# Performance work log

Hardware: AMD Instinct MI355X
Metric: run time of the kernel (lower is better)

The kernel has to match this reference:

```python
import jax, jax.numpy as jnp
import numpy as np

D = 128      # dim_emb
FF = 512     # dim_ff
H = 8        # nb_heads
HD = D // H
NLE = 2      # encoder layers (action and state)
NLD = 2      # decoder layers
NS = 1       # num_state_encoder
TANH_CLIP = 10.0
BIG = jnp.float32(1e9)


def layer_norm(h, g, b):
    mu = jnp.mean(h, -1, keepdims=True)
    v = jnp.var(h, -1, keepdims=True)
    return g * (h - mu) * jax.lax.rsqrt(v + 1e-5) + b


def mha_self(h, Wq, Wk, Wv, Wo, bq, bk, bv, bo):
    B, S, _ = h.shape
    q = (h @ Wq + bq).reshape(B, S, H, HD)
    k = (h @ Wk + bk).reshape(B, S, H, HD)
    v = (h @ Wv + bv).reshape(B, S, H, HD)
    a = jax.nn.softmax(jnp.einsum('bqhd,bkhd->bhqk', q, k) / np.float32(np.sqrt(HD)), axis=-1)
    return jnp.einsum('bhqk,bkhd->bqhd', a, v).reshape(B, S, D) @ Wo + bo


def encode(tok, Wemb, bemb, aW, aB, W1, b1, W2, b2, ln):
    # tok: [B, S, 2] raw coordinates -> [B, S, D]
    h = tok @ Wemb + bemb
    for l in range(NLE):
        h = layer_norm(h + mha_self(h, *aW[l], *aB[l]), ln[l, 0, 0], ln[l, 0, 1])
        ffo = jax.nn.relu(h @ W1[l] + b1[l]) @ W2[l] + b2[l]
        h = layer_norm(h + ffo, ln[l, 1, 0], ln[l, 1, 1])
    return h


def _forward(x, start_idx, action_k, state_k,
             a_emb_W, a_emb_b, a_attn_W, a_attn_b, a_ff_W1, a_ff_b1, a_ff_W2, a_ff_b2, a_ln,
             s_emb_W, s_emb_b, s_attn_W, s_attn_b, s_ff_W1, s_ff_b1, s_ff_W2, s_ff_b2, s_ln,
             WK, bK, WV, bV, Wq_mlp, bq_mlp, d_Wq, d_bq, d_Wo, d_bo):
    B, N, _ = x.shape
    bar = jnp.arange(B)
    first = x[bar, start_idx]                                   # [B,2]
    mask0 = jnp.ones((B, N), bool).at[bar, start_idx].set(False)  # True = unvisited
    ka, ks = action_k, state_k

    def step(carry, _):
        mask, last_idx, logp = carry
        last = x[bar, last_idx]                                  # [B,2]
        # knn over unvisited nodes (visited nodes pushed to distance BIG)
        d2 = jnp.sum((x - last[:, None, :]) ** 2, -1)
        d2 = jnp.where(mask, d2, BIG)
        _, knn_idx = jax.lax.top_k(-d2, ks)                      # [B,ks] nearest-first global node ids
        aidx = knn_idx[:, :ka]                                   # [B,ka]
        valid = mask[bar[:, None], aidx]                         # unvisited -> valid action
        # action encoder: k_action neighbors + last visited node
        tok_a = jnp.concatenate([x[bar[:, None], aidx], last[:, None, :]], 1)       # [B,ka+1,2]
        emb_a = encode(tok_a, a_emb_W, a_emb_b, a_attn_W, a_attn_b, a_ff_W1, a_ff_b1, a_ff_W2, a_ff_b2, a_ln)
        emb_q = emb_a[:, ka]
        emb_o = emb_a[:, :ka]
        # state encoder: k_state neighbors + last + first visited node
        tok_s = jnp.concatenate([x[bar[:, None], knn_idx], last[:, None, :], first[:, None, :]], 1)  # [B,ks+2,2]
        emb_s = encode(tok_s, s_emb_W, s_emb_b, s_attn_W, s_attn_b, s_ff_W1, s_ff_b1, s_ff_W2, s_ff_b2, s_ln)
        emb_q = jnp.concatenate([emb_q, emb_s[:, ks], emb_s[:, ks + 1]], -1)        # [B,(2*NS+1)*D]
        emb_o = jnp.concatenate([emb_o, emb_s[:, :ka]], -1)                          # [B,ka,(NS+1)*D]
        # decoder: per-layer K/V slices, masked cross-attention, final tanh-clipped pointer
        h = emb_q @ Wq_mlp + bq_mlp                              # [B,D]
        K = (emb_o @ WK + bK).reshape(B, ka, NLD, D)
        V = (emb_o @ WV + bV).reshape(B, ka, NLD, D)
        for l in range(NLD - 1):
            q = (h @ d_Wq[l] + d_bq[l]).reshape(B, H, HD)
            kk = K[:, :, l].reshape(B, ka, H, HD)
            vv = V[:, :, l].reshape(B, ka, H, HD)
            sc = jnp.einsum('bhd,bkhd->bhk', q, kk) / np.float32(np.sqrt(HD))
            sc = jnp.where(valid[:, None, :], sc, -BIG)
            o = jnp.einsum('bhk,bkhd->bhd', jax.nn.softmax(sc, -1), vv).reshape(B, D) @ d_Wo[l] + d_bo[l]
            h = h + o
        q = h @ d_Wq[NLD - 1] + d_bq[NLD - 1]
        logits = TANH_CLIP * jnp.tanh(jnp.einsum('bd,bkd->bk', q, K[:, :, NLD - 1]) / np.float32(np.sqrt(D)))
        logits = jnp.where(valid, logits, -BIG)
        prob = jax.nn.softmax(logits, -1)
        idx = jnp.argmax(prob, 1)                                # deterministic choice
        nxt = aidx[bar, idx]
        logp = logp + jnp.log(prob[bar, idx])
        mask = mask.at[bar, nxt].set(False)
        return (mask, nxt, logp), nxt

    (_, _, logp), ys = jax.lax.scan(step, (mask0, start_idx, jnp.zeros(B, jnp.float32)), None, length=N - 1)
    tours = jnp.concatenate([start_idx[:, None], ys.T], 1)       # [B,N]
    return tours, logp


def setup_inputs() -> dict:
    key = jax.random.key(0)
    ks = jax.random.split(key, 16)
    def Nrm(k, shape, fan):
        return jax.random.normal(k, shape, jnp.float32) / np.float32(np.sqrt(fan))
    B, Nn = 64, 50
    inp = {}
    inp['x'] = jax.random.uniform(ks[0], (B, Nn, 2), jnp.float32)
    inp['start_idx'] = jax.random.randint(ks[1], (B,), 0, Nn)
    inp['action_k'] = 15
    inp['state_k'] = 35
    inp['a_emb_W'] = Nrm(ks[2], (2, D), 2); inp['a_emb_b'] = jnp.zeros((D,))
    inp['a_attn_W'] = Nrm(ks[3], (NLE, 4, D, D), D); inp['a_attn_b'] = jnp.zeros((NLE, 4, D))
    inp['a_ff_W1'] = Nrm(ks[4], (NLE, D, FF), D); inp['a_ff_b1'] = jnp.zeros((NLE, FF))
    inp['a_ff_W2'] = Nrm(ks[5], (NLE, FF, D), FF); inp['a_ff_b2'] = jnp.zeros((NLE, D))
    inp['a_ln'] = jnp.stack([jnp.ones((NLE, 2, D)), jnp.zeros((NLE, 2, D))], 2)
    inp['s_emb_W'] = Nrm(ks[6], (2, D), 2); inp['s_emb_b'] = jnp.zeros((D,))
    inp['s_attn_W'] = Nrm(ks[7], (NLE, 4, D, D), D); inp['s_attn_b'] = jnp.zeros((NLE, 4, D))
    inp['s_ff_W1'] = Nrm(ks[8], (NLE, D, FF), D); inp['s_ff_b1'] = jnp.zeros((NLE, FF))
    inp['s_ff_W2'] = Nrm(ks[9], (NLE, FF, D), FF); inp['s_ff_b2'] = jnp.zeros((NLE, D))
    inp['s_ln'] = jnp.stack([jnp.ones((NLE, 2, D)), jnp.zeros((NLE, 2, D))], 2)
    inp['WK'] = Nrm(ks[10], ((NS + 1) * D, NLD * D), (NS + 1) * D); inp['bK'] = jnp.zeros((NLD * D,))
    inp['WV'] = Nrm(ks[11], ((NS + 1) * D, NLD * D), (NS + 1) * D); inp['bV'] = jnp.zeros((NLD * D,))
    inp['Wq_mlp'] = Nrm(ks[12], ((2 * NS + 1) * D, D), (2 * NS + 1) * D); inp['bq_mlp'] = jnp.zeros((D,))
    inp['d_Wq'] = Nrm(ks[13], (NLD, D, D), D); inp['d_bq'] = jnp.zeros((NLD, D))
    inp['d_Wo'] = Nrm(ks[14], (NLD, D, D), D); inp['d_bo'] = jnp.zeros((NLD, D))
    return inp


def reference(x, start_idx, action_k, state_k,
              a_emb_W, a_emb_b, a_attn_W, a_attn_b, a_ff_W1, a_ff_b1, a_ff_W2, a_ff_b2, a_ln,
              s_emb_W, s_emb_b, s_attn_W, s_attn_b, s_ff_W1, s_ff_b1, s_ff_W2, s_ff_b2, s_ln,
              WK, bK, WV, bV, Wq_mlp, bq_mlp, d_Wq, d_bq, d_Wo, d_bo):
    return _forward(x, start_idx, action_k, state_k,
                    a_emb_W, a_emb_b, a_attn_W, a_attn_b, a_ff_W1, a_ff_b1, a_ff_W2, a_ff_b2, a_ln,
                    s_emb_W, s_emb_b, s_attn_W, s_attn_b, s_ff_W1, s_ff_b1, s_ff_W2, s_ff_b2, s_ln,
                    WK, bK, WV, bV, Wq_mlp, bq_mlp, d_Wq, d_bq, d_Wo, d_bo)
```

## Files before the change

### kernel.cpp

```cpp
#include <hip/hip_runtime.h>

namespace {

constexpr int NB  = 64;
constexpr int NN  = 50;
constexpr int DM  = 128;
constexpr int FFDIM = 512;
constexpr int NHD = 8;
constexpr int HDM = 16;
constexpr int KA  = 15;
constexpr int KS  = 35;
constexpr int TA  = 16;
constexpr int TS  = 37;
constexpr int NT  = 1024;
constexpr float BIGF = 1000000000.0f;

constexpr int OFF_HA  = 0;
constexpr int OFF_HS  = 2048;
constexpr int OFF_SCR = 6784;
constexpr int SCR_FLOATS = 28416;
constexpr int SMEM_FLOATS = OFF_SCR + SCR_FLOATS;
constexpr int SMEM_BYTES  = SMEM_FLOATS * 4;

struct Params {
  const float* x; const int* start;
  const float* a_emb_W; const float* a_emb_b;
  const float* a_attn_W; const float* a_attn_b;
  const float* a_ff_W1; const float* a_ff_b1;
  const float* a_ff_W2; const float* a_ff_b2;
  const float* a_ln;
  const float* s_emb_W; const float* s_emb_b;
  const float* s_attn_W; const float* s_attn_b;
  const float* s_ff_W1; const float* s_ff_b1;
  const float* s_ff_W2; const float* s_ff_b2;
  const float* s_ln;
  const float* WK; const float* bK;
  const float* WV; const float* bV;
  const float* Wq_mlp; const float* bq_mlp;
  const float* d_Wq; const float* d_bq;
  const float* d_Wo; const float* d_bo;
  float* out;
};

template<int R>
__device__ inline void fma4(float4* acc, const float* __restrict__ in, const int* ro, int kb,
                            float4 w0, float4 w1, float4 w2, float4 w3)
{
#pragma unroll
  for (int i = 0; i < R; ++i) {
    float4 a = *(const float4*)(in + ro[i] + kb);
    acc[i].x = fmaf(a.x,w0.x,acc[i].x); acc[i].y = fmaf(a.x,w0.y,acc[i].y);
    acc[i].z = fmaf(a.x,w0.z,acc[i].z); acc[i].w = fmaf(a.x,w0.w,acc[i].w);
    acc[i].x = fmaf(a.y,w1.x,acc[i].x); acc[i].y = fmaf(a.y,w1.y,acc[i].y);
    acc[i].z = fmaf(a.y,w1.z,acc[i].z); acc[i].w = fmaf(a.y,w1.w,acc[i].w);
    acc[i].x = fmaf(a.z,w2.x,acc[i].x); acc[i].y = fmaf(a.z,w2.y,acc[i].y);
    acc[i].z = fmaf(a.z,w2.z,acc[i].z); acc[i].w = fmaf(a.z,w2.w,acc[i].w);
    acc[i].x = fmaf(a.w,w3.x,acc[i].x); acc[i].y = fmaf(a.w,w3.y,acc[i].y);
    acc[i].z = fmaf(a.w,w3.z,acc[i].z); acc[i].w = fmaf(a.w,w3.w,acc[i].w);
  }
}

template<int R, int NG, int NM, int K>
__device__ inline void matmul_blk(const float* __restrict__ in, int lda,
                                  const float* __restrict__ W, int ldw, int wBlk,
                                  const float* __restrict__ bias,
                                  float* __restrict__ out, int ldo, int outBlk,
                                  int T, bool relu, int tid, int tid0)
{
  constexpr int NACT = NG * NM * 32;
  const int t = tid - tid0;
  if (t < 0 || t >= NACT) return;
  const int cw = t % (NM * 32);
  const int g  = t / (NM * 32);
  const int m  = cw >> 5;
  const int c  = (cw & 31) << 2;
  const float* __restrict__ wp = W + (size_t)m * wBlk + c;
  float* __restrict__ op = out + (size_t)m * outBlk + c;
  const int rb = g * R;
  int ro[R];
#pragma unroll
  for (int i = 0; i < R; ++i) ro[i] = min(rb + i, T - 1) * lda;
  float4 acc[R];
  if (bias) {
    const float4 bv4 = *(const float4*)(bias + m * 128 + c);
#pragma unroll
    for (int i = 0; i < R; ++i) acc[i] = bv4;
  } else {
#pragma unroll
    for (int i = 0; i < R; ++i) acc[i] = make_float4(0.f, 0.f, 0.f, 0.f);
  }
  float4 wA0, wA1, wA2, wA3, wB0, wB1, wB2, wB3;
  wA0 = *(const float4*)(wp + (size_t)0 * ldw);
  wA1 = *(const float4*)(wp + (size_t)1 * ldw);
  wA2 = *(const float4*)(wp + (size_t)2 * ldw);
  wA3 = *(const float4*)(wp + (size_t)3 * ldw);
#pragma unroll 1
  for (int kk = 0; kk < K; kk += 8) {
    wB0 = *(const float4*)(wp + (size_t)(kk + 4) * ldw);
    wB1 = *(const float4*)(wp + (size_t)(kk + 5) * ldw);
    wB2 = *(const float4*)(wp + (size_t)(kk + 6) * ldw);
    wB3 = *(const float4*)(wp + (size_t)(kk + 7) * ldw);
    fma4<R>(acc, in, ro, kk, wA0, wA1, wA2, wA3);
    if (kk + 8 < K) {
      wA0 = *(const float4*)(wp + (size_t)(kk +  8) * ldw);
      wA1 = *(const float4*)(wp + (size_t)(kk +  9) * ldw);
      wA2 = *(const float4*)(wp + (size_t)(kk + 10) * ldw);
      wA3 = *(const float4*)(wp + (size_t)(kk + 11) * ldw);
    }
    fma4<R>(acc, in, ro, kk + 4, wB0, wB1, wB2, wB3);
  }
#pragma unroll
  for (int i = 0; i < R; ++i) {
    if (rb + i < T) {
      float4 r2 = acc[i];
      if (relu) {
        r2.x = fmaxf(r2.x, 0.f); r2.y = fmaxf(r2.y, 0.f);
        r2.z = fmaxf(r2.z, 0.f); r2.w = fmaxf(r2.w, 0.f);
      }
      *(float4*)(op + (rb + i) * ldo) = r2;
    }
  }
}

__device__ inline void matvec128(const float* __restrict__ in, const float* __restrict__ W,
                                 const float* __restrict__ bias, float* __restrict__ out,
                                 int K, float* __restrict__ red, int tid)
{
  const int c = tid & 127;
  const int s = tid >> 7;
  const int ks = K >> 3;
  const int k0 = s * ks;
  float acc = 0.f;
#pragma unroll 8
  for (int k = k0; k < k0 + ks; ++k) acc = fmaf(in[k], W[(size_t)k * 128 + c], acc);
  red[tid] = acc;
  __syncthreads();
  if (tid < 128) {
    float sum = ((red[c] + red[128 + c]) + (red[256 + c] + red[384 + c]))
              + ((red[512 + c] + red[640 + c]) + (red[768 + c] + red[896 + c]));
    out[c] = bias[c] + sum;
  }
  __syncthreads();
}

__device__ inline void layernorm_add2(float* __restrict__ h, const float* __restrict__ a1,
                                      const float* __restrict__ a2,
                                      const float* __restrict__ g, const float* __restrict__ bta,
                                      int T, int tid)
{
  const int lane = tid & 63;
  const int wvl = tid >> 6;
  for (int r = wvl; r < T; r += NT / 64) {
    float v0 = h[r * DM + lane]      + a1[r * DM + lane];
    float v1 = h[r * DM + lane + 64] + a1[r * DM + lane + 64];
    if (a2) { v0 += a2[r * DM + lane]; v1 += a2[r * DM + lane + 64]; }
    float sum = v0 + v1;
    for (int off = 32; off; off >>= 1) sum += __shfl_xor(sum, off);
    float mu = sum * (1.0f / 128.0f);
    float d0 = v0 - mu, d1 = v1 - mu;
    float sq = d0 * d0 + d1 * d1;
    for (int off = 32; off; off >>= 1) sq += __shfl_xor(sq, off);
    float rs = 1.0f / sqrtf(sq * (1.0f / 128.0f) + 1e-5f);
    h[r * DM + lane]      = g[lane]      * d0 * rs + bta[lane];
    h[r * DM + lane + 64] = g[lane + 64] * d1 * rs + bta[lane + 64];
  }
}

template<int T, int R, int NG>
__device__ void encode_block(float* __restrict__ h, float* __restrict__ scr,
                             const float* __restrict__ tok,
                             const float* __restrict__ embW, const float* __restrict__ embB,
                             const float* __restrict__ attnW, const float* __restrict__ attnB,
                             const float* __restrict__ W1, const float* __restrict__ b1,
                             const float* __restrict__ W2, const float* __restrict__ b2,
                             const float* __restrict__ ln, int tid)
{
  const int lane = tid & 63;
  const int wvl = tid >> 6;
  constexpr int TT = T * T;
  float* q = scr;
  float* k = scr + T * DM;
  float* v = scr + 2 * T * DM;
  float* s = scr + 3 * T * DM;
  for (int idx = tid; idx < T * DM; idx += NT) {
    int r = idx >> 7, c = idx & 127;
    h[idx] = tok[2 * r] * embW[c] + tok[2 * r + 1] * embW[DM + c] + embB[c];
  }
  __syncthreads();
  for (int l = 0; l < 2; ++l) {
    const float* Wq = attnW + (size_t)(l * 4) * DM * DM;
    const float* bq = attnB + (l * 4) * DM;
    matmul_blk<R, NG, 3, DM>(h, DM, Wq, DM, DM * DM, bq, q, DM, T * DM, T, false, tid, 0);
    __syncthreads();
    for (int idx = tid; idx < NHD * TT; idx += NT) {
      int hd = idx / TT; int rem = idx - hd * TT; int i = rem / T; int j = rem - i * T;
      const float4* q4 = (const float4*)(q + i * DM + hd * HDM);
      const float4* k4 = (const float4*)(k + j * DM + hd * HDM);
      float acc = 0.f;
#pragma unroll
      for (int d = 0; d < 4; ++d) {
        float4 qa = q4[d], ka = k4[d];
        acc += qa.x * ka.x + qa.y * ka.y + qa.z * ka.z + qa.w * ka.w;
      }
      s[idx] = acc * 0.25f;
    }
    __syncthreads();
    for (int r = wvl; r < NHD * T; r += NT / 64) {
      float val = (lane < T) ? s[r * T + lane] : -INFINITY;
      float mx = val;
      for (int off = 32; off; off >>= 1) mx = fmaxf(mx, __shfl_xor(mx, off));
      float e = (lane < T) ? expf(val - mx) : 0.f;
      float sum = e;
      for (int off = 32; off; off >>= 1) sum += __shfl_xor(sum, off);
      if (lane < T) s[r * T + lane] = e / sum;
    }
    __syncthreads();
    for (int idx = tid; idx < T * DM; idx += NT) {
      int i = idx >> 7, c = idx & 127; int hd = c >> 4;
      const float* ar = s + (hd * T + i) * T;
      float acc = 0.f;
#pragma unroll 4
      for (int j = 0; j < T; ++j) acc = fmaf(ar[j], v[j * DM + c], acc);
      q[idx] = acc;
    }
    __syncthreads();
    matmul_blk<R, NG, 1, DM>(q, DM, Wq + (size_t)3 * DM * DM, DM, 0, bq + 3 * DM,
                             v, DM, 0, T, false, tid, 0);
    __syncthreads();
    layernorm_add2(h, v, nullptr, ln + ((l * 2 + 0) * 2 + 0) * DM, ln + ((l * 2 + 0) * 2 + 1) * DM, T, tid);
    __syncthreads();
    const float* W1l = W1 + (size_t)l * DM * FFDIM;
    const float* b1l = b1 + l * FFDIM;
    const float* W2l = W2 + (size_t)l * FFDIM * DM;
    float* hidden = scr;
    float* ff2o   = scr + T * FFDIM;
    float* ff2b   = ff2o + T * DM;
    matmul_blk<R, NG, 4, DM>(h, DM, W1l, FFDIM, 128, b1l, hidden, FFDIM, 128, T, true, tid, 0);
    __syncthreads();
    matmul_blk<R, NG, 1, 256>(hidden, FFDIM, W2l, DM, 0, b2 + l * DM,
                              ff2o, DM, 0, T, false, tid, 0);
    matmul_blk<R, NG, 1, 256>(hidden + 256, FFDIM, W2l + (size_t)256 * DM, DM, 0, nullptr,
                              ff2b, DM, 0, T, false, tid, 256);
    __syncthreads();
    layernorm_add2(h, ff2o, ff2b, ln + ((l * 2 + 1) * 2 + 0) * DM, ln + ((l * 2 + 1) * 2 + 1) * DM, T, tid);
    __syncthreads();
  }
}

__global__ __launch_bounds__(NT)
void tsp_kernel(Params p)
{
  const int b = blockIdx.x;
  const int tid = threadIdx.x;
  const int lane = tid & 63;
  const int wv = tid >> 6;

  extern __shared__ float sm[];
  float* hA  = sm + OFF_HA;
  float* hS  = sm + OFF_HS;
  float* scr = sm + OFF_SCR;

  __shared__ float xl[NN * 2];
  __shared__ int   maskS[NN];
  __shared__ int   knnS[KS];
  __shared__ int   validS[KA];
  __shared__ float d2S[NN];
  __shared__ float tokA[TA * 2];
  __shared__ float tokS[TS * 2];
  __shared__ int   lastS;
  __shared__ float logpS;

  for (int i = tid; i < NN * 2; i += NT) xl[i] = p.x[b * NN * 2 + i];
  const int st = p.start[b];
  for (int i = tid; i < NN; i += NT) maskS[i] = (i != st) ? 1 : 0;
  if (tid == 0) {
    lastS = st; logpS = 0.f;
    p.out[b * NN] = (float)st;
  }
  __syncthreads();
  const float fx = xl[2 * st], fy = xl[2 * st + 1];

  for (int t = 0; t < NN - 1; ++t) {
    const int last = lastS;
    const float lx = xl[2 * last], ly = xl[2 * last + 1];

    for (int j = tid; j < NN; j += NT) {
      float dx = __fsub_rn(xl[2 * j], lx);
      float dy = __fsub_rn(xl[2 * j + 1], ly);
      float dd = __fadd_rn(__fmul_rn(dx, dx), __fmul_rn(dy, dy));
      d2S[j] = maskS[j] ? dd : BIGF;
    }
    __syncthreads();

    if (wv == 0) {
      float v = (lane < NN) ? d2S[lane] : 2.0f * BIGF;
      const int vi = lane;
      for (int s2 = 0; s2 < KS; ++s2) {
        float mv = v; int mi = vi;
        for (int off = 32; off; off >>= 1) {
          float ov = __shfl_xor(mv, off);
          int oi = __shfl_xor(mi, off);
          if (ov < mv || (ov == mv && oi < mi)) { mv = ov; mi = oi; }
        }
        if (lane == 0) knnS[s2] = mi;
        if (vi == mi) v = 4.0f * BIGF;
      }
    }
    __syncthreads();

    if (tid < KA) validS[tid] = maskS[knnS[tid]];
    if (tid < KS) { int j = knnS[tid]; tokS[2 * tid] = xl[2 * j]; tokS[2 * tid + 1] = xl[2 * j + 1]; }
    if (tid < KA) { int j = knnS[tid]; tokA[2 * tid] = xl[2 * j]; tokA[2 * tid + 1] = xl[2 * j + 1]; }
    if (tid == NT - 1) { tokA[2 * KA] = lx; tokA[2 * KA + 1] = ly; }
    if (tid == NT - 2) { tokS[2 * KS] = lx; tokS[2 * KS + 1] = ly; }
    if (tid == NT - 3) { tokS[2 * KS + 2] = fx; tokS[2 * KS + 3] = fy; }
    __syncthreads();

    encode_block<TA, 4, 4>(hA, scr, tokA, p.a_emb_W, p.a_emb_b, p.a_attn_W, p.a_attn_b,
                           p.a_ff_W1, p.a_ff_b1, p.a_ff_W2, p.a_ff_b2, p.a_ln, tid);
    encode_block<TS, 8, 5>(hS, scr, tokS, p.s_emb_W, p.s_emb_b, p.s_attn_W, p.s_attn_b,
                           p.s_ff_W1, p.s_ff_b1, p.s_ff_W2, p.s_ff_b2, p.s_ln, tid);

    float* embq = scr;
    float* embo = scr + 384;
    float* Kd   = scr + 4224;
    float* Vd   = scr + 8064;
    float* hdec = scr + 11904;
    float* qd   = scr + 12032;
    float* scd  = scr + 12160;
    float* od   = scr + 12288;
    float* tmp  = scr + 12416;
    float* red  = scr + 12544;

    if (tid < 384) {
      embq[tid] = (tid < 128) ? hA[KA * DM + tid]
                : (tid < 256) ? hS[KS * DM + (tid - 128)]
                              : hS[(KS + 1) * DM + (tid - 256)];
    }
    for (int idx = tid; idx < KA * 256; idx += NT) {
      int r = idx >> 8, c = idx & 255;
      embo[idx] = (c < 128) ? hA[r * DM + c] : hS[r * DM + (c - 128)];
    }
    __syncthreads();

    matmul_blk<8, 2, 2, 256>(embo, 256, p.WK, 256, 128, p.bK, Kd, 256, 128, KA, false, tid, 0);
    matmul_blk<8, 2, 2, 256>(embo, 256, p.WV, 256, 128, p.bV, Vd, 256, 128, KA, false, tid, 128);
    matvec128(embq, p.Wq_mlp, p.bq_mlp, hdec, 384, red, tid);

    matvec128(hdec, p.d_Wq, p.d_bq, qd, DM, red, tid);
    if (tid < NHD * KA) {
      int hd = tid / KA, kk2 = tid - hd * KA;
      const float* qh = qd + hd * HDM;
      const float* kh = Kd + kk2 * 256 + hd * HDM;
      float acc = 0.f;
#pragma unroll
      for (int d = 0; d < HDM; ++d) acc += qh[d] * kh[d];
      acc = acc / 4.0f;
      scd[tid] = validS[kk2] ? acc : -BIGF;
    }
    __syncthreads();
    if (tid < NHD) {
      float mx = -INFINITY;
#pragma unroll
      for (int kk2 = 0; kk2 < KA; ++kk2) mx = fmaxf(mx, scd[tid * KA + kk2]);
      float e[KA]; float sum = 0.f;
#pragma unroll
      for (int kk2 = 0; kk2 < KA; ++kk2) { e[kk2] = expf(scd[tid * KA + kk2] - mx); sum += e[kk2]; }
      float inv = 1.0f / sum;
#pragma unroll
      for (int kk2 = 0; kk2 < KA; ++kk2) scd[tid * KA + kk2] = e[kk2] * inv;
    }
    __syncthreads();
    if (tid < DM) {
      int hd = tid >> 4;
      float acc = 0.f;
#pragma unroll
      for (int kk2 = 0; kk2 < KA; ++kk2) acc = fmaf(scd[hd * KA + kk2], Vd[kk2 * 256 + tid], acc);
      od[tid] = acc;
    }
    __syncthreads();
    matvec128(od, p.d_Wo, p.d_bo, tmp, DM, red, tid);
    if (tid < DM) hdec[tid] += tmp[tid];
    __syncthreads();

    matvec128(hdec, p.d_Wq + DM * DM, p.d_bq + DM, qd, DM, red, tid);
    if (wv == 0) {
      float lg = -BIGF;
      if (lane < KA) {
        const float* kf = Kd + lane * 256 + 128;
        float acc = 0.f;
#pragma unroll 8
        for (int d = 0; d < DM; ++d) acc = fmaf(qd[d], kf[d], acc);
        acc = acc / 11.313708498984761f;
        lg = validS[lane] ? 10.0f * tanhf(acc) : -BIGF;
      }
      float mv = lg; int mi = (lane < KA) ? lane : 1000;
      for (int off = 32; off; off >>= 1) {
        float ov = __shfl_xor(mv, off);
        int oi = __shfl_xor(mi, off);
        if (ov > mv || (ov == mv && oi < mi)) { mv = ov; mi = oi; }
      }
      float e = (lane < KA) ? expf(lg - mv) : 0.f;
      float sum = e;
      for (int off = 32; off; off >>= 1) sum += __shfl_xor(sum, off);
      if (lane == 0) {
        int nxt = knnS[mi];
        logpS += -logf(sum);
        maskS[nxt] = 0;
        lastS = nxt;
        p.out[b * NN + t + 1] = (float)nxt;
      }
    }
    __syncthreads();
  }

  if (tid == 0) p.out[NB * NN + b] = logpS;
}

}

extern "C" void kernel_launch(void* const* d_in, const int* in_sizes, int n_in,
                              void* d_out, int out_size, void* d_ws, size_t ws_size,
                              hipStream_t stream)
{
  (void)in_sizes; (void)n_in; (void)out_size; (void)d_ws; (void)ws_size;
  Params p;
  p.x        = (const float*)d_in[0];
  p.start    = (const int*)d_in[1];
  p.a_emb_W  = (const float*)d_in[4];
  p.a_emb_b  = (const float*)d_in[5];
  p.a_attn_W = (const float*)d_in[6];
  p.a_attn_b = (const float*)d_in[7];
  p.a_ff_W1  = (const float*)d_in[8];
  p.a_ff_b1  = (const float*)d_in[9];
  p.a_ff_W2  = (const float*)d_in[10];
  p.a_ff_b2  = (const float*)d_in[11];
  p.a_ln     = (const float*)d_in[12];
  p.s_emb_W  = (const float*)d_in[13];
  p.s_emb_b  = (const float*)d_in[14];
  p.s_attn_W = (const float*)d_in[15];
  p.s_attn_b = (const float*)d_in[16];
  p.s_ff_W1  = (const float*)d_in[17];
  p.s_ff_b1  = (const float*)d_in[18];
  p.s_ff_W2  = (const float*)d_in[19];
  p.s_ff_b2  = (const float*)d_in[20];
  p.s_ln     = (const float*)d_in[21];
  p.WK       = (const float*)d_in[22];
  p.bK       = (const float*)d_in[23];
  p.WV       = (const float*)d_in[24];
  p.bV       = (const float*)d_in[25];
  p.Wq_mlp   = (const float*)d_in[26];
  p.bq_mlp   = (const float*)d_in[27];
  p.d_Wq     = (const float*)d_in[28];
  p.d_bq     = (const float*)d_in[29];
  p.d_Wo     = (const float*)d_in[30];
  p.d_bo     = (const float*)d_in[31];
  p.out      = (float*)d_out;

  (void)hipFuncSetAttribute((const void*)tsp_kernel,
                            hipFuncAttributeMaxDynamicSharedMemorySize, SMEM_BYTES);
  tsp_kernel<<<NB, NT, SMEM_BYTES, stream>>>(p);
}
```

Baseline: 43.83 ms.

## Stage weight slabs in LDS for encoder matmuls and halve block size

Replaces the register-streamed global weight matmul with one that cooperatively loads K-slabs of the weight matrix into shared memory, then has every thread compute a row-group by column tile from the staged slab. The block size drops from 1024 to 512 threads, and the per-layer row-tiling parameters and the split FF2 reduction are retuned to fit. This aims to cut redundant global weight reads across row groups and to raise per-thread work. The cost is an extra barrier on every slab, and fewer threads to hide latency in the serial per-step loop.

```diff
diff --git a/kernel.cpp b/kernel.cpp
--- a/kernel.cpp
+++ b/kernel.cpp
@@ -12,13 +12,13 @@
 constexpr int KS  = 35;
 constexpr int TA  = 16;
 constexpr int TS  = 37;
-constexpr int NT  = 1024;
+constexpr int NT  = 512;
 constexpr float BIGF = 1000000000.0f;
 
 constexpr int OFF_HA  = 0;
 constexpr int OFF_HS  = 2048;
 constexpr int OFF_SCR = 6784;
-constexpr int SCR_FLOATS = 28416;
+constexpr int SCR_FLOATS = 27776;
 constexpr int SMEM_FLOATS = OFF_SCR + SCR_FLOATS;
 constexpr int SMEM_BYTES  = SMEM_FLOATS * 4;
 
@@ -42,72 +42,61 @@
   float* out;
 };
 
-template<int R>
-__device__ inline void fma4(float4* acc, const float* __restrict__ in, const int* ro, int kb,
-                            float4 w0, float4 w1, float4 w2, float4 w3)
-{
-#pragma unroll
-  for (int i = 0; i < R; ++i) {
-    float4 a = *(const float4*)(in + ro[i] + kb);
-    acc[i].x = fmaf(a.x,w0.x,acc[i].x); acc[i].y = fmaf(a.x,w0.y,acc[i].y);
-    acc[i].z = fmaf(a.x,w0.z,acc[i].z); acc[i].w = fmaf(a.x,w0.w,acc[i].w);
-    acc[i].x = fmaf(a.y,w1.x,acc[i].x); acc[i].y = fmaf(a.y,w1.y,acc[i].y);
-    acc[i].z = fmaf(a.y,w1.z,acc[i].z); acc[i].w = fmaf(a.y,w1.w,acc[i].w);
-    acc[i].x = fmaf(a.z,w2.x,acc[i].x); acc[i].y = fmaf(a.z,w2.y,acc[i].y);
-    acc[i].z = fmaf(a.z,w2.z,acc[i].z); acc[i].w = fmaf(a.z,w2.w,acc[i].w);
-    acc[i].x = fmaf(a.w,w3.x,acc[i].x); acc[i].y = fmaf(a.w,w3.y,acc[i].y);
-    acc[i].z = fmaf(a.w,w3.z,acc[i].z); acc[i].w = fmaf(a.w,w3.w,acc[i].w);
-  }
-}
-
-template<int R, int NG, int NM, int K>
-__device__ inline void matmul_blk(const float* __restrict__ in, int lda,
+template<int C, int CB, int KB, int R, int K>
+__device__ inline void matmul_lds(const float* __restrict__ in, int lda,
                                   const float* __restrict__ W, int ldw, int wBlk,
                                   const float* __restrict__ bias,
-                                  float* __restrict__ out, int ldo, int outBlk,
-                                  int T, bool relu, int tid, int tid0)
-{
-  constexpr int NACT = NG * NM * 32;
-  const int t = tid - tid0;
-  if (t < 0 || t >= NACT) return;
-  const int cw = t % (NM * 32);
-  const int g  = t / (NM * 32);
-  const int m  = cw >> 5;
-  const int c  = (cw & 31) << 2;
-  const float* __restrict__ wp = W + (size_t)m * wBlk + c;
-  float* __restrict__ op = out + (size_t)m * outBlk + c;
+                                  float* __restrict__ out, int ldo, int oBlk,
+                                  float* __restrict__ wbuf, int T, bool relu, int tid)
+{
+  constexpr int W4  = C >> 2;
+  constexpr int C4B = CB >> 2;
+  constexpr int NSL = K / KB;
+  const int cw = tid % W4;
+  const int g  = tid / W4;
+  const int m  = cw / C4B;
+  const int ci = (cw % C4B) * 4;
   const int rb = g * R;
   int ro[R];
 #pragma unroll
   for (int i = 0; i < R; ++i) ro[i] = min(rb + i, T - 1) * lda;
   float4 acc[R];
-  if (bias) {
-    const float4 bv4 = *(const float4*)(bias + m * 128 + c);
-#pragma unroll
-    for (int i = 0; i < R; ++i) acc[i] = bv4;
-  } else {
-#pragma unroll
-    for (int i = 0; i < R; ++i) acc[i] = make_float4(0.f, 0.f, 0.f, 0.f);
-  }
-  float4 wA0, wA1, wA2, wA3, wB0, wB1, wB2, wB3;
-  wA0 = *(const float4*)(wp + (size_t)0 * ldw);
-  wA1 = *(const float4*)(wp + (size_t)1 * ldw);
-  wA2 = *(const float4*)(wp + (size_t)2 * ldw);
-  wA3 = *(const float4*)(wp + (size_t)3 * ldw);
-#pragma unroll 1
-  for (int kk = 0; kk < K; kk += 8) {
-    wB0 = *(const float4*)(wp + (size_t)(kk + 4) * ldw);
-    wB1 = *(const float4*)(wp + (size_t)(kk + 5) * ldw);
-    wB2 = *(const float4*)(wp + (size_t)(kk + 6) * ldw);
-    wB3 = *(const float4*)(wp + (size_t)(kk + 7) * ldw);
-    fma4<R>(acc, in, ro, kk, wA0, wA1, wA2, wA3);
-    if (kk + 8 < K) {
-      wA0 = *(const float4*)(wp + (size_t)(kk +  8) * ldw);
-      wA1 = *(const float4*)(wp + (size_t)(kk +  9) * ldw);
-      wA2 = *(const float4*)(wp + (size_t)(kk + 10) * ldw);
-      wA3 = *(const float4*)(wp + (size_t)(kk + 11) * ldw);
-    }
-    fma4<R>(acc, in, ro, kk + 4, wB0, wB1, wB2, wB3);
+  {
+    const float4 bv = *(const float4*)(bias + m * CB + ci);
+#pragma unroll
+    for (int i = 0; i < R; ++i) acc[i] = bv;
+  }
+#define FMA16_(aa, i) \
+  acc[i].x = fmaf((aa).x,w0.x,acc[i].x); acc[i].y = fmaf((aa).x,w0.y,acc[i].y); \
+  acc[i].z = fmaf((aa).x,w0.z,acc[i].z); acc[i].w = fmaf((aa).x,w0.w,acc[i].w); \
+  acc[i].x = fmaf((aa).y,w1.x,acc[i].x); acc[i].y = fmaf((aa).y,w1.y,acc[i].y); \
+  acc[i].z = fmaf((aa).y,w1.z,acc[i].z); acc[i].w = fmaf((aa).y,w1.w,acc[i].w); \
+  acc[i].x = fmaf((aa).z,w2.x,acc[i].x); acc[i].y = fmaf((aa).z,w2.y,acc[i].y); \
+  acc[i].z = fmaf((aa).z,w2.z,acc[i].z); acc[i].w = fmaf((aa).z,w2.w,acc[i].w); \
+  acc[i].x = fmaf((aa).w,w3.x,acc[i].x); acc[i].y = fmaf((aa).w,w3.y,acc[i].y); \
+  acc[i].z = fmaf((aa).w,w3.z,acc[i].z); acc[i].w = fmaf((aa).w,w3.w,acc[i].w);
+  for (int sl = 0; sl < NSL; ++sl) {
+    __syncthreads();
+    for (int i = tid; i < KB * W4; i += NT) {
+      const int kk = i / W4, cc = i % W4;
+      const int mm = cc / C4B, cci = (cc % C4B) * 4;
+      *(float4*)(wbuf + (size_t)i * 4) =
+        *(const float4*)(W + (size_t)mm * wBlk + (size_t)(sl * KB + kk) * ldw + cci);
+    }
+    __syncthreads();
+    const int kbase = sl * KB;
+#pragma unroll 2
+    for (int kk = 0; kk < KB; kk += 4) {
+      float4 w0 = *(const float4*)(wbuf + (size_t)(kk + 0) * W4 * 4 + cw * 4);
+      float4 w1 = *(const float4*)(wbuf + (size_t)(kk + 1) * W4 * 4 + cw * 4);
+      float4 w2 = *(const float4*)(wbuf + (size_t)(kk + 2) * W4 * 4 + cw * 4);
+      float4 w3 = *(const float4*)(wbuf + (size_t)(kk + 3) * W4 * 4 + cw * 4);
+#pragma unroll
+      for (int i = 0; i < R; ++i) {
+        float4 a = *(const float4*)(in + ro[i] + kbase + kk);
+        FMA16_(a, i);
+      }
+    }
   }
 #pragma unroll
   for (int i = 0; i < R; ++i) {
@@ -117,9 +106,10 @@
         r2.x = fmaxf(r2.x, 0.f); r2.y = fmaxf(r2.y, 0.f);
         r2.z = fmaxf(r2.z, 0.f); r2.w = fmaxf(r2.w, 0.f);
       }
-      *(float4*)(op + (rb + i) * ldo) = r2;
-    }
-  }
+      *(float4*)(out + (size_t)m * oBlk + (size_t)(rb + i) * ldo + ci) = r2;
+    }
+  }
+#undef FMA16_
 }
 
 __device__ inline void matvec128(const float* __restrict__ in, const float* __restrict__ W,
@@ -128,32 +118,26 @@
 {
   const int c = tid & 127;
   const int s = tid >> 7;
-  const int ks = K >> 3;
+  const int ks = K >> 2;
   const int k0 = s * ks;
   float acc = 0.f;
 #pragma unroll 8
   for (int k = k0; k < k0 + ks; ++k) acc = fmaf(in[k], W[(size_t)k * 128 + c], acc);
   red[tid] = acc;
   __syncthreads();
-  if (tid < 128) {
-    float sum = ((red[c] + red[128 + c]) + (red[256 + c] + red[384 + c]))
-              + ((red[512 + c] + red[640 + c]) + (red[768 + c] + red[896 + c]));
-    out[c] = bias[c] + sum;
-  }
+  if (tid < 128) out[c] = bias[c] + ((red[c] + red[128 + c]) + (red[256 + c] + red[384 + c]));
   __syncthreads();
 }
 
-__device__ inline void layernorm_add2(float* __restrict__ h, const float* __restrict__ a1,
-                                      const float* __restrict__ a2,
-                                      const float* __restrict__ g, const float* __restrict__ bta,
-                                      int T, int tid)
+__device__ inline void layernorm_add(float* __restrict__ h, const float* __restrict__ a1,
+                                     const float* __restrict__ g, const float* __restrict__ bta,
+                                     int T, int tid)
 {
   const int lane = tid & 63;
   const int wvl = tid >> 6;
   for (int r = wvl; r < T; r += NT / 64) {
     float v0 = h[r * DM + lane]      + a1[r * DM + lane];
     float v1 = h[r * DM + lane + 64] + a1[r * DM + lane + 64];
-    if (a2) { v0 += a2[r * DM + lane]; v1 += a2[r * DM + lane + 64]; }
     float sum = v0 + v1;
     for (int off = 32; off; off >>= 1) sum += __shfl_xor(sum, off);
     float mu = sum * (1.0f / 128.0f);
@@ -166,7 +150,7 @@
   }
 }
 
-template<int T, int R, int NG>
+template<int T, int RQKV, int RC, int RFF>
 __device__ void encode_block(float* __restrict__ h, float* __restrict__ scr,
                              const float* __restrict__ tok,
                              const float* __restrict__ embW, const float* __restrict__ embB,
@@ -186,11 +170,11 @@
     int r = idx >> 7, c = idx & 127;
     h[idx] = tok[2 * r] * embW[c] + tok[2 * r + 1] * embW[DM + c] + embB[c];
   }
-  __syncthreads();
   for (int l = 0; l < 2; ++l) {
-    const float* Wq = attnW + (size_t)(l * 4) * DM * DM;
-    const float* bq = attnB + (l * 4) * DM;
-    matmul_blk<R, NG, 3, DM>(h, DM, Wq, DM, DM * DM, bq, q, DM, T * DM, T, false, tid, 0);
+    const float* Wl = attnW + (size_t)(l * 4) * DM * DM;
+    const float* bl = attnB + (l * 4) * DM;
+    matmul_lds<384, 128, 32, RQKV, 128>(h, DM, Wl, DM, DM * DM, bl,
+                                        q, DM, T * DM, s, T, false, tid);
     __syncthreads();
     for (int idx = tid; idx < NHD * TT; idx += NT) {
       int hd = idx / TT; int rem = idx - hd * TT; int i = rem / T; int j = rem - i * T;
@@ -223,31 +207,27 @@
       for (int j = 0; j < T; ++j) acc = fmaf(ar[j], v[j * DM + c], acc);
       q[idx] = acc;
     }
-    __syncthreads();
-    matmul_blk<R, NG, 1, DM>(q, DM, Wq + (size_t)3 * DM * DM, DM, 0, bq + 3 * DM,
-                             v, DM, 0, T, false, tid, 0);
-    __syncthreads();
-    layernorm_add2(h, v, nullptr, ln + ((l * 2 + 0) * 2 + 0) * DM, ln + ((l * 2 + 0) * 2 + 1) * DM, T, tid);
-    __syncthreads();
+    matmul_lds<128, 128, 64, RC, 128>(q, DM, Wl + (size_t)3 * DM * DM, DM, 0, bl + 3 * DM,
+                                      v, DM, 0, s, T, false, tid);
+    __syncthreads();
+    layernorm_add(h, v, ln + ((l * 2 + 0) * 2 + 0) * DM, ln + ((l * 2 + 0) * 2 + 1) * DM, T, tid);
     const float* W1l = W1 + (size_t)l * DM * FFDIM;
-    const float* b1l = b1 + l * FFDIM;
     const float* W2l = W2 + (size_t)l * FFDIM * DM;
     float* hidden = scr;
-    float* ff2o   = scr + T * FFDIM;
-    float* ff2b   = ff2o + T * DM;
-    matmul_blk<R, NG, 4, DM>(h, DM, W1l, FFDIM, 128, b1l, hidden, FFDIM, 128, T, true, tid, 0);
-    __syncthreads();
-    matmul_blk<R, NG, 1, 256>(hidden, FFDIM, W2l, DM, 0, b2 + l * DM,
-                              ff2o, DM, 0, T, false, tid, 0);
-    matmul_blk<R, NG, 1, 256>(hidden + 256, FFDIM, W2l + (size_t)256 * DM, DM, 0, nullptr,
-                              ff2b, DM, 0, T, false, tid, 256);
-    __syncthreads();
-    layernorm_add2(h, ff2o, ff2b, ln + ((l * 2 + 1) * 2 + 0) * DM, ln + ((l * 2 + 1) * 2 + 1) * DM, T, tid);
-    __syncthreads();
-  }
-}
-
-__global__ __launch_bounds__(NT)
+    float* slab1  = scr + T * FFDIM;
+    float* ff2o   = scr + T * FFDIM + 32 * DM;
+    matmul_lds<512, 512, 16, RFF, 128>(h, DM, W1l, FFDIM, 0, b1 + l * FFDIM,
+                                       hidden, FFDIM, 0, slab1, T, true, tid);
+    __syncthreads();
+    matmul_lds<128, 128, 32, RC, 512>(hidden, FFDIM, W2l, DM, 0, b2 + l * DM,
+                                      ff2o, DM, 0, slab1, T, false, tid);
+    __syncthreads();
+    layernorm_add(h, ff2o, ln + ((l * 2 + 1) * 2 + 0) * DM, ln + ((l * 2 + 1) * 2 + 1) * DM, T, tid);
+    __syncthreads();
+  }
+}
+
+__global__ __launch_bounds__(NT, 1)
 void tsp_kernel(Params p)
 {
   const int b = blockIdx.x;
@@ -316,10 +296,10 @@
     if (tid == NT - 3) { tokS[2 * KS + 2] = fx; tokS[2 * KS + 3] = fy; }
     __syncthreads();
 
-    encode_block<TA, 4, 4>(hA, scr, tokA, p.a_emb_W, p.a_emb_b, p.a_attn_W, p.a_attn_b,
-                           p.a_ff_W1, p.a_ff_b1, p.a_ff_W2, p.a_ff_b2, p.a_ln, tid);
-    encode_block<TS, 8, 5>(hS, scr, tokS, p.s_emb_W, p.s_emb_b, p.s_attn_W, p.s_attn_b,
-                           p.s_ff_W1, p.s_ff_b1, p.s_ff_W2, p.s_ff_b2, p.s_ln, tid);
+    encode_block<TA, 4, 1, 4>(hA, scr, tokA, p.a_emb_W, p.a_emb_b, p.a_attn_W, p.a_attn_b,
+                              p.a_ff_W1, p.a_ff_b1, p.a_ff_W2, p.a_ff_b2, p.a_ln, tid);
+    encode_block<TS, 8, 3, 10>(hS, scr, tokS, p.s_emb_W, p.s_emb_b, p.s_attn_W, p.s_attn_b,
+                               p.s_ff_W1, p.s_ff_b1, p.s_ff_W2, p.s_ff_b2, p.s_ln, tid);
 
     float* embq = scr;
     float* embo = scr + 384;
@@ -331,6 +311,7 @@
     float* od   = scr + 12288;
     float* tmp  = scr + 12416;
     float* red  = scr + 12544;
+    float* slabD= scr + 13568;
 
     if (tid < 384) {
       embq[tid] = (tid < 128) ? hA[KA * DM + tid]
@@ -341,10 +322,11 @@
       int r = idx >> 8, c = idx & 255;
       embo[idx] = (c < 128) ? hA[r * DM + c] : hS[r * DM + (c - 128)];
     }
-    __syncthreads();
-
-    matmul_blk<8, 2, 2, 256>(embo, 256, p.WK, 256, 128, p.bK, Kd, 256, 128, KA, false, tid, 0);
-    matmul_blk<8, 2, 2, 256>(embo, 256, p.WV, 256, 128, p.bV, Vd, 256, 128, KA, false, tid, 128);
+    matmul_lds<256, 256, 32, 2, 256>(embo, 256, p.WK, 256, 0, p.bK,
+                                     Kd, 256, 0, slabD, KA, false, tid);
+    matmul_lds<256, 256, 32, 2, 256>(embo, 256, p.WV, 256, 0, p.bV,
+                                     Vd, 256, 0, slabD, KA, false, tid);
+    __syncthreads();
     matvec128(embq, p.Wq_mlp, p.bq_mlp, hdec, 384, red, tid);
 
     matvec128(hdec, p.d_Wq, p.d_bq, qd, DM, red, tid);
```

Result: slower. 97.98 ms (+123.6%).
